# Performance work log

Measured on AMD Instinct MI355X. Metric: run time of the kernel, lower is better.

## Reference

```python
import jax, jax.numpy as jnp
import numpy as np

EMBED = 1024
HEADS = 16
HEAD_DIM = EMBED // HEADS
LN_EPS = 1e-5


def setup_inputs() -> dict:
    key = jax.random.key(0)
    ks = jax.random.split(key, 12)
    B, LQ, LK = 2, 2048, 2048
    s = 1.0 / np.sqrt(EMBED)
    inp = {
        "query_seq": jax.random.normal(ks[0], (B, LQ, EMBED), jnp.float32),
        "key_value_seq": jax.random.normal(ks[1], (B, LK, EMBED), jnp.float32),
        "prompt_size": 0,
        "Wq": jax.random.normal(ks[2], (EMBED, EMBED), jnp.float32) * s,
        "bq": jnp.zeros((EMBED,), jnp.float32),
        "Wk": jax.random.normal(ks[3], (EMBED, EMBED), jnp.float32) * s,
        "bk": jnp.zeros((EMBED,), jnp.float32),
        "Wv": jax.random.normal(ks[4], (EMBED, EMBED), jnp.float32) * s,
        "bv": jnp.zeros((EMBED,), jnp.float32),
        "Wo": jax.random.normal(ks[5], (EMBED, EMBED), jnp.float32) * s,
        "bo": jnp.zeros((EMBED,), jnp.float32),
        "ln_gamma": jnp.ones((EMBED,), jnp.float32),
        "ln_beta": jnp.zeros((EMBED,), jnp.float32),
    }
    return inp


def _split_heads(x):
    B, L, _ = x.shape
    return x.reshape(B, L, HEADS, HEAD_DIM).transpose(0, 2, 1, 3)  # [B,H,L,Dh]


def reference(query_seq, key_value_seq, prompt_size, Wq, bq, Wk, bk, Wv, bv, Wo, bo, ln_gamma, ln_beta):
    # projections (torch nn.Linear: x @ W.T + b)
    q = _split_heads(query_seq @ Wq.T + bq)
    k = _split_heads(key_value_seq @ Wk.T + bk)
    v = _split_heads(key_value_seq @ Wv.T + bv)
    # naive attention: full score matrix, softmax over keys
    scores = jnp.einsum("bhqd,bhkd->bhqk", q, k) / np.sqrt(HEAD_DIM).astype(np.float32)
    attn = jax.nn.softmax(scores, axis=-1)
    ctx = jnp.einsum("bhqk,bhkd->bhqd", attn, v)
    B, H, LQ, Dh = ctx.shape
    ctx = ctx.transpose(0, 2, 1, 3).reshape(B, LQ, H * Dh)
    out = ctx @ Wo.T + bo
    # residual + LayerNorm
    x = out + query_seq
    mu = jnp.mean(x, axis=-1, keepdims=True)
    var = jnp.var(x, axis=-1, keepdims=True)
    return (x - mu) * jax.lax.rsqrt(var + LN_EPS) * ln_gamma + ln_beta
```

## Files before the change

### kernel.cpp

```cpp
#include <hip/hip_runtime.h>

typedef unsigned short u16;
typedef unsigned int u32;
typedef __attribute__((ext_vector_type(8))) __bf16 bf16x8;
typedef __attribute__((ext_vector_type(4))) float f32x4;
typedef __attribute__((ext_vector_type(16))) float f32x16;

#define EMBED 1024
#define NB 2
#define LQ 2048
#define HEADS 16
#define DH 64
#define QSCALE 0.18033688011112042f

__device__ __forceinline__ u16 f2bf(float f) {
  u32 u = __float_as_uint(f);
  u32 r = (u + 0x7FFFu + ((u >> 16) & 1u)) >> 16;
  return (u16)r;
}

__device__ __forceinline__ void glds16(const void* g, void* l) {
  __builtin_amdgcn_global_load_lds((const __attribute__((address_space(1))) void*)g,
                                   (__attribute__((address_space(3))) void*)l, 16, 0, 0);
}

__device__ __forceinline__ f32x4 mfma16(bf16x8 a, bf16x8 b, f32x4 c) {
  return __builtin_amdgcn_mfma_f32_16x16x32_bf16(a, b, c, 0, 0, 0);
}
__device__ __forceinline__ f32x16 mfma32(bf16x8 a, bf16x8 b, f32x16 c) {
  return __builtin_amdgcn_mfma_f32_32x32x16_bf16(a, b, c, 0, 0, 0);
}

__device__ __forceinline__ void pl32(u32& a, u32& b) {
  asm("v_permlane32_swap_b32 %0, %1" : "+v"(a), "+v"(b));
}

__device__ __forceinline__ u32 packbf(float a, float b) {
  return __builtin_amdgcn_perm(__float_as_uint(b), __float_as_uint(a), 0x07060302u);
}

__global__ __launch_bounds__(256) void cast_kernel(
    const float* __restrict__ q, const float* __restrict__ kv,
    const float* __restrict__ wq, const float* __restrict__ wk,
    const float* __restrict__ wv, const float* __restrict__ wo,
    u16* __restrict__ qb, u16* __restrict__ kvb, u16* __restrict__ wqb,
    u16* __restrict__ wkb, u16* __restrict__ wvb, u16* __restrict__ wob) {
  int bid = blockIdx.x;
  const float* src;
  u16* dst;
  long base;
  if (bid < 2048) {
    src = q; dst = qb; base = (long)bid * 2048;
  } else if (bid < 4096) {
    src = kv; dst = kvb; base = (long)(bid - 2048) * 2048;
  } else {
    int wsel = (bid - 4096) >> 9;
    int wb = (bid - 4096) & 511;
    if (wsel == 0) { src = wq; dst = wqb; }
    else if (wsel == 1) { src = wk; dst = wkb; }
    else if (wsel == 2) { src = wv; dst = wvb; }
    else { src = wo; dst = wob; }
    base = (long)wb * 2048;
  }
  long e = base + (long)threadIdx.x * 8;
  float4 f0 = *(const float4*)(src + e);
  float4 f1 = *(const float4*)(src + e + 4);
  uint4 o;
  o.x = (u32)f2bf(f0.x) | ((u32)f2bf(f0.y) << 16);
  o.y = (u32)f2bf(f0.z) | ((u32)f2bf(f0.w) << 16);
  o.z = (u32)f2bf(f1.x) | ((u32)f2bf(f1.y) << 16);
  o.w = (u32)f2bf(f1.z) | ((u32)f2bf(f1.w) << 16);
  *(uint4*)(dst + e) = o;
}

template <int IT>
__device__ __forceinline__ void gemm_core(
    u16* As, u16* Bs, const u16* __restrict__ A, const u16* __restrict__ W,
    const float* __restrict__ bias, const float* __restrict__ resid,
    void* __restrict__ outp, int mode, int bx, int by) {
  const int K = EMBED;
  const int TM = IT * 32;
  const int tid = threadIdx.x;
  const int lane = tid & 63;
  const int wv = tid >> 6;
  const int wm = wv >> 1, wn = wv & 1;
  const int l16 = lane & 15, quad = lane >> 4;
  const long tile_m = (long)bx * TM;
  const long tile_n = (long)by * 128;

  f32x4 z4 = {0.f, 0.f, 0.f, 0.f};
  f32x4 acc[IT][4];
#pragma unroll
  for (int i = 0; i < IT; i++)
#pragma unroll
    for (int j = 0; j < 4; j++) acc[i][j] = z4;

  for (int k0 = 0; k0 < K; k0 += 64) {
#pragma unroll
    for (int it = 0; it < TM / 32; it++) {
      int lin = it * 256 + tid;
      int row = lin >> 3, cc = lin & 7;
      glds16(A + (tile_m + row) * K + k0 + ((cc ^ (row & 7)) << 3), As + lin * 8);
    }
#pragma unroll
    for (int it = 0; it < 4; it++) {
      int lin = it * 256 + tid;
      int row = lin >> 3, cc = lin & 7;
      glds16(W + (tile_n + row) * K + k0 + ((cc ^ (row & 7)) << 3), Bs + lin * 8);
    }
    __syncthreads();
#pragma unroll
    for (int ki = 0; ki < 2; ki++) {
      bf16x8 af[IT], bfr[4];
#pragma unroll
      for (int i = 0; i < IT; i++) {
        int row = wm * (IT * 16) + i * 16 + l16;
        af[i] = *(const bf16x8*)(As + row * 64 + (((ki * 4 + quad) ^ (row & 7)) << 3));
      }
#pragma unroll
      for (int j = 0; j < 4; j++) {
        int row = wn * 64 + j * 16 + l16;
        bfr[j] = *(const bf16x8*)(Bs + row * 64 + (((ki * 4 + quad) ^ (row & 7)) << 3));
      }
#pragma unroll
      for (int i = 0; i < IT; i++)
#pragma unroll
        for (int j = 0; j < 4; j++) acc[i][j] = mfma16(af[i], bfr[j], acc[i][j]);
    }
    __syncthreads();
  }

#pragma unroll
  for (int j = 0; j < 4; j++) {
    int gn = (int)tile_n + wn * 64 + j * 16 + l16;
    float bv = bias[gn];
#pragma unroll
    for (int i = 0; i < IT; i++) {
      long gm0 = tile_m + wm * (IT * 16) + i * 16 + quad * 4;
      if (mode == 3) {
#pragma unroll
        for (int r = 0; r < 4; r++) {
          long idx = (gm0 + r) * EMBED + gn;
          ((float*)outp)[idx] = acc[i][j][r] + bv + resid[idx];
        }
      } else if (mode == 2) {
        int b = (int)(gm0 >> 11), l = (int)(gm0 & 2047);
        int hh = gn >> 6, dh = gn & 63;
        uint2 pk;
        pk.x = (u32)f2bf(acc[i][j][0] + bv) | ((u32)f2bf(acc[i][j][1] + bv) << 16);
        pk.y = (u32)f2bf(acc[i][j][2] + bv) | ((u32)f2bf(acc[i][j][3] + bv) << 16);
        *(uint2*)((u16*)outp + (long)((b * HEADS + hh) * DH + dh) * LQ + l) = pk;
      } else {
#pragma unroll
        for (int r = 0; r < 4; r++) {
          long gm = gm0 + r;
          float v = acc[i][j][r] + bv;
          if (mode == 0) v *= QSCALE;
          int b = (int)(gm >> 11), l = (int)(gm & 2047);
          int hh = gn >> 6, dh = gn & 63;
          ((u16*)outp)[(long)((b * HEADS + hh) * LQ + l) * DH + dh] = f2bf(v);
        }
      }
    }
  }
}

__global__ __launch_bounds__(256, 4) void qkv_kernel(
    const u16* __restrict__ qb, const u16* __restrict__ kvb,
    const u16* __restrict__ wqb, const u16* __restrict__ wkb, const u16* __restrict__ wvb,
    const float* __restrict__ bq, const float* __restrict__ bk, const float* __restrict__ bv,
    u16* __restrict__ Qh, u16* __restrict__ Kh, u16* __restrict__ Vt) {
  __shared__ u16 As[64 * 64];
  __shared__ u16 Bs[128 * 64];
  if (blockIdx.z == 0)      gemm_core<2>(As, Bs, qb,  wqb, bq, nullptr, Qh, 0, blockIdx.x, blockIdx.y);
  else if (blockIdx.z == 1) gemm_core<2>(As, Bs, kvb, wkb, bk, nullptr, Kh, 1, blockIdx.x, blockIdx.y);
  else                      gemm_core<2>(As, Bs, kvb, wvb, bv, nullptr, Vt, 2, blockIdx.x, blockIdx.y);
}

__global__ __launch_bounds__(256, 4) void oproj_kernel(
    const u16* __restrict__ ctx, const u16* __restrict__ wob,
    const float* __restrict__ bo, const float* __restrict__ resid, float* __restrict__ out) {
  __shared__ u16 As[64 * 64];
  __shared__ u16 Bs[128 * 64];
  gemm_core<2>(As, Bs, ctx, wob, bo, resid, out, 3, blockIdx.x, blockIdx.y);
}

__global__ __launch_bounds__(256, 2) void attn_kernel(
    const u16* __restrict__ Qh, const u16* __restrict__ Kh,
    const u16* __restrict__ Vt, u16* __restrict__ ctx) {
  __shared__ u16 KVs[4][2][64 * 64];
  const int tid = threadIdx.x;
  const int lane = tid & 63;
  const int wv = tid >> 6;
  const int l32 = lane & 31, h = lane >> 5;
  const int qt = blockIdx.x, bh = blockIdx.y;
  const long qoff = (long)bh * (LQ * DH) + (long)qt * (128 * DH);
  const long koff = (long)bh * (LQ * DH);
  const long voff = (long)bh * (DH * LQ);
  const int qbase = wv * 32;

#define STAGE_KV(t, N)                                                          \
  do {                                                                          \
    _Pragma("unroll") for (int it = 0; it < 2; it++) {                          \
      int lin = it * 256 + tid;                                                 \
      int row = lin >> 3, cc = lin & 7;                                         \
      glds16(Kh + koff + (long)((t) * 64 + row) * 64 + ((cc ^ (row & 7)) << 3), \
             &KVs[N][0][0] + lin * 8);                                          \
      glds16(Vt + voff + (long)row * LQ + (t) * 64 + ((cc ^ (row & 7)) << 3),   \
             &KVs[N][1][0] + lin * 8);                                          \
    }                                                                           \
  } while (0)

#define SYNC(W)                                                                 \
  do {                                                                          \
    asm volatile("s_waitcnt vmcnt(" #W ")" ::: "memory");                       \
    __builtin_amdgcn_s_barrier();                                               \
    asm volatile("" ::: "memory");                                              \
  } while (0)

  bf16x8 bq[4];
  {
    const u16* qp = Qh + qoff + (qbase + l32) * 64 + h * 8;
#pragma unroll
    for (int ks = 0; ks < 4; ks++) bq[ks] = *(const bf16x8*)(qp + ks * 16);
  }

  STAGE_KV(0, 0);
  STAGE_KV(1, 1);
  STAGE_KV(2, 2);
  SYNC(4);

  f32x16 z16 = {0.f, 0.f, 0.f, 0.f, 0.f, 0.f, 0.f, 0.f,
                0.f, 0.f, 0.f, 0.f, 0.f, 0.f, 0.f, 0.f};
  f32x16 ot[2];
  ot[0] = z16;
  ot[1] = z16;
  f32x16 st[2];
  uint2 pk[2][4];
  float2 ls2 = {0.f, 0.f};

#define DO_S(C)                                                                  \
  do {                                                                           \
    __builtin_amdgcn_s_setprio(1);                                               \
    _Pragma("unroll") for (int ks = 0; ks < 4; ks++) {                           \
      _Pragma("unroll") for (int mt = 0; mt < 2; mt++) {                         \
        int row = mt * 32 + l32;                                                 \
        bf16x8 ak = *(const bf16x8*)(&KVs[C][0][0] + row * 64 +                  \
                                     (((ks * 2 + h) ^ (row & 7)) << 3));         \
        st[mt] = mfma32(ak, bq[ks], (ks == 0) ? z16 : st[mt]);                   \
      }                                                                          \
    }                                                                            \
    __builtin_amdgcn_s_setprio(0);                                               \
  } while (0)

#define DO_SM()                                                                  \
  do {                                                                           \
    _Pragma("unroll") for (int mt = 0; mt < 2; mt++) {                           \
      _Pragma("unroll") for (int g = 0; g < 4; g++) {                            \
        float p0 = __builtin_amdgcn_exp2f(st[mt][g * 4 + 0]);                    \
        float p1 = __builtin_amdgcn_exp2f(st[mt][g * 4 + 1]);                    \
        float p2 = __builtin_amdgcn_exp2f(st[mt][g * 4 + 2]);                    \
        float p3 = __builtin_amdgcn_exp2f(st[mt][g * 4 + 3]);                    \
        ls2.x += p0 + p2;                                                        \
        ls2.y += p1 + p3;                                                        \
        pk[mt][g].x = packbf(p0, p1);                                            \
        pk[mt][g].y = packbf(p2, p3);                                            \
      }                                                                          \
    }                                                                            \
  } while (0)

#define DO_PV(P)                                                                 \
  do {                                                                           \
    _Pragma("unroll") for (int s = 0; s < 4; s++) {                              \
      uint2 wa = pk[s >> 1][(s & 1) * 2];                                        \
      uint2 wb = pk[s >> 1][(s & 1) * 2 + 1];                                    \
      u32 a0 = wa.x, b0 = wb.x, a1 = wa.y, b1 = wb.y;                            \
      pl32(a0, b0);                                                              \
      pl32(a1, b1);                                                              \
      union { u32 u[4]; bf16x8 v; } bp;                                          \
      bp.u[0] = a0;                                                              \
      bp.u[1] = a1;                                                              \
      bp.u[2] = b0;                                                              \
      bp.u[3] = b1;                                                              \
      __builtin_amdgcn_s_setprio(1);                                             \
      _Pragma("unroll") for (int mt2 = 0; mt2 < 2; mt2++) {                      \
        int row = mt2 * 32 + l32;                                                \
        bf16x8 av = *(const bf16x8*)(&KVs[P][1][0] + row * 64 +                  \
                                     ((((s << 1) + h) ^ (row & 7)) << 3));       \
        ot[mt2] = mfma32(av, bp.v, ot[mt2]);                                     \
      }                                                                          \
      __builtin_amdgcn_s_setprio(0);                                             \
    }                                                                            \
  } while (0)

#define AITER(kt, P, C, N, W)                                                    \
  do {                                                                           \
    if ((kt) + 2 < 32) STAGE_KV((kt) + 2, N);                                    \
    DO_SM();                                                                     \
    DO_S(C);                                                                     \
    DO_PV(P);                                                                    \
    SYNC(W);                                                                     \
  } while (0)

  DO_S(0);

  AITER(1, 0, 1, 3, 4);
  for (int k0 = 2; k0 < 30; k0 += 4) {
    AITER(k0 + 0, 1, 2, 0, 4);
    AITER(k0 + 1, 2, 3, 1, 4);
    AITER(k0 + 2, 3, 0, 2, 4);
    AITER(k0 + 3, 0, 1, 3, 4);
  }
  AITER(30, 1, 2, 0, 0);
  AITER(31, 2, 3, 1, 0);
  DO_SM();
  DO_PV(3);

#undef STAGE_KV
#undef SYNC
#undef DO_S
#undef DO_SM
#undef DO_PV
#undef AITER

  float lsum = ls2.x + ls2.y;
  lsum += __shfl_xor(lsum, 32);
  float inv = 1.0f / lsum;

  const int b = bh >> 4, head = bh & 15;
  int qrow = qt * 128 + qbase + l32;
  long base = (long)(b * LQ + qrow) * EMBED + head * DH;
#pragma unroll
  for (int mt = 0; mt < 2; mt++) {
#pragma unroll
    for (int g = 0; g < 4; g++) {
      uint2 pkk;
      pkk.x = (u32)f2bf(ot[mt][g * 4 + 0] * inv) | ((u32)f2bf(ot[mt][g * 4 + 1] * inv) << 16);
      pkk.y = (u32)f2bf(ot[mt][g * 4 + 2] * inv) | ((u32)f2bf(ot[mt][g * 4 + 3] * inv) << 16);
      *(uint2*)(ctx + base + mt * 32 + g * 8 + 4 * h) = pkk;
    }
  }
}

__global__ __launch_bounds__(256) void ln_kernel(
    float* __restrict__ x, const float* __restrict__ gamma, const float* __restrict__ beta) {
  __shared__ float red[8];
  const int tid = threadIdx.x;
  const long row = blockIdx.x;
  float4 v = *(const float4*)(x + row * EMBED + tid * 4);
  float s = v.x + v.y + v.z + v.w;
  float sq = v.x * v.x + v.y * v.y + v.z * v.z + v.w * v.w;
#pragma unroll
  for (int off = 1; off < 64; off <<= 1) {
    s += __shfl_xor(s, off);
    sq += __shfl_xor(sq, off);
  }
  if ((tid & 63) == 0) {
    red[(tid >> 6) * 2] = s;
    red[(tid >> 6) * 2 + 1] = sq;
  }
  __syncthreads();
  s = red[0] + red[2] + red[4] + red[6];
  sq = red[1] + red[3] + red[5] + red[7];
  float mu = s * (1.f / EMBED);
  float var = sq * (1.f / EMBED) - mu * mu;
  float rstd = rsqrtf(var + 1e-5f);
  float4 g = *(const float4*)(gamma + tid * 4);
  float4 bt = *(const float4*)(beta + tid * 4);
  float4 ov;
  ov.x = (v.x - mu) * rstd * g.x + bt.x;
  ov.y = (v.y - mu) * rstd * g.y + bt.y;
  ov.z = (v.z - mu) * rstd * g.z + bt.z;
  ov.w = (v.w - mu) * rstd * g.w + bt.w;
  *(float4*)(x + row * EMBED + tid * 4) = ov;
}

extern "C" void kernel_launch(void* const* d_in, const int* in_sizes, int n_in,
                              void* d_out, int out_size, void* d_ws, size_t ws_size,
                              hipStream_t stream) {
  const float* q     = (const float*)d_in[0];
  const float* kv    = (const float*)d_in[1];
  const float* Wq    = (const float*)d_in[3];
  const float* bq    = (const float*)d_in[4];
  const float* Wk    = (const float*)d_in[5];
  const float* bk    = (const float*)d_in[6];
  const float* Wv    = (const float*)d_in[7];
  const float* bv    = (const float*)d_in[8];
  const float* Wo    = (const float*)d_in[9];
  const float* bo    = (const float*)d_in[10];
  const float* gamma = (const float*)d_in[11];
  const float* beta  = (const float*)d_in[12];

  char* ws = (char*)d_ws;
  u16* qb  = (u16*)(ws + (0l  << 20));
  u16* kvb = (u16*)(ws + (8l  << 20));
  u16* wqb = (u16*)(ws + (16l << 20));
  u16* wkb = (u16*)(ws + (18l << 20));
  u16* wvb = (u16*)(ws + (20l << 20));
  u16* wob = (u16*)(ws + (22l << 20));
  u16* Qh  = (u16*)(ws + (24l << 20));
  u16* Kh  = (u16*)(ws + (32l << 20));
  u16* Vt  = (u16*)(ws + (40l << 20));
  u16* ctx = (u16*)(ws + (48l << 20));
  float* out = (float*)d_out;

  cast_kernel<<<6144, 256, 0, stream>>>(q, kv, Wq, Wk, Wv, Wo, qb, kvb, wqb, wkb, wvb, wob);
  qkv_kernel<<<dim3(64, 8, 3), 256, 0, stream>>>(qb, kvb, wqb, wkb, wvb, bq, bk, bv, Qh, Kh, Vt);
  attn_kernel<<<dim3(16, 32), 256, 0, stream>>>(Qh, Kh, Vt, ctx);
  oproj_kernel<<<dim3(64, 8), 256, 0, stream>>>(ctx, wob, bo, q, out);
  ln_kernel<<<4096, 256, 0, stream>>>(out, gamma, beta);
}
```

Measured before the change: 207.7 us.

## Batch LDS loads and interleave softmax with QK MFMAs in attention loop

The attention inner loop now loads all K and V fragments from LDS into registers up front. It splits the score MFMA and the exp/pack softmax work by half-tile, so exp on one half can overlap MFMAs on the other, and it issues all PV MFMAs back to back. The launch grid is also flattened to 1D with a block-index swizzle, so blocks that land on the same XCD share the same batch-head K/V. This costs more VGPRs for the buffered fragments, which could hurt occupancy at the current launch bounds of 2 blocks per CU.

```diff
diff --git a/kernel.cpp b/kernel.cpp
--- a/kernel.cpp
+++ b/kernel.cpp
@@ -193,7 +193,9 @@
   const int lane = tid & 63;
   const int wv = tid >> 6;
   const int l32 = lane & 31, h = lane >> 5;
-  const int qt = blockIdx.x, bh = blockIdx.y;
+  const int bid = (int)blockIdx.x;
+  const int swz = (bid & 7) * 64 + (bid >> 3);
+  const int bh = swz >> 4, qt = swz & 15;
   const long qoff = (long)bh * (LQ * DH) + (long)qt * (128 * DH);
   const long koff = (long)bh * (LQ * DH);
   const long voff = (long)bh * (DH * LQ);
@@ -237,39 +239,54 @@
   ot[1] = z16;
   f32x16 st[2];
   uint2 pk[2][4];
+  bf16x8 ak[4][2], av[4][2], bpv[4];
   float2 ls2 = {0.f, 0.f};
 
-#define DO_S(C)                                                                  \
-  do {                                                                           \
-    __builtin_amdgcn_s_setprio(1);                                               \
+#define LOAD_K(C)                                                                \
+  do {                                                                           \
     _Pragma("unroll") for (int ks = 0; ks < 4; ks++) {                           \
       _Pragma("unroll") for (int mt = 0; mt < 2; mt++) {                         \
         int row = mt * 32 + l32;                                                 \
-        bf16x8 ak = *(const bf16x8*)(&KVs[C][0][0] + row * 64 +                  \
-                                     (((ks * 2 + h) ^ (row & 7)) << 3));         \
-        st[mt] = mfma32(ak, bq[ks], (ks == 0) ? z16 : st[mt]);                   \
+        ak[ks][mt] = *(const bf16x8*)(&KVs[C][0][0] + row * 64 +                 \
+                                      (((ks * 2 + h) ^ (row & 7)) << 3));        \
       }                                                                          \
     }                                                                            \
-    __builtin_amdgcn_s_setprio(0);                                               \
-  } while (0)
-
-#define DO_SM()                                                                  \
-  do {                                                                           \
-    _Pragma("unroll") for (int mt = 0; mt < 2; mt++) {                           \
-      _Pragma("unroll") for (int g = 0; g < 4; g++) {                            \
-        float p0 = __builtin_amdgcn_exp2f(st[mt][g * 4 + 0]);                    \
-        float p1 = __builtin_amdgcn_exp2f(st[mt][g * 4 + 1]);                    \
-        float p2 = __builtin_amdgcn_exp2f(st[mt][g * 4 + 2]);                    \
-        float p3 = __builtin_amdgcn_exp2f(st[mt][g * 4 + 3]);                    \
-        ls2.x += p0 + p2;                                                        \
-        ls2.y += p1 + p3;                                                        \
-        pk[mt][g].x = packbf(p0, p1);                                            \
-        pk[mt][g].y = packbf(p2, p3);                                            \
+  } while (0)
+
+#define LOAD_V(P)                                                                \
+  do {                                                                           \
+    _Pragma("unroll") for (int s = 0; s < 4; s++) {                              \
+      _Pragma("unroll") for (int mt2 = 0; mt2 < 2; mt2++) {                      \
+        int row = mt2 * 32 + l32;                                                \
+        av[s][mt2] = *(const bf16x8*)(&KVs[P][1][0] + row * 64 +                 \
+                                      ((((s << 1) + h) ^ (row & 7)) << 3));      \
       }                                                                          \
     }                                                                            \
   } while (0)
 
-#define DO_PV(P)                                                                 \
+#define DO_S_H(MT)                                                               \
+  do {                                                                           \
+    __builtin_amdgcn_s_setprio(1);                                               \
+    _Pragma("unroll") for (int ks = 0; ks < 4; ks++)                             \
+        st[MT] = mfma32(ak[ks][MT], bq[ks], (ks == 0) ? z16 : st[MT]);           \
+    __builtin_amdgcn_s_setprio(0);                                               \
+  } while (0)
+
+#define DO_SM_H(MT)                                                              \
+  do {                                                                           \
+    _Pragma("unroll") for (int g = 0; g < 4; g++) {                              \
+      float p0 = __builtin_amdgcn_exp2f(st[MT][g * 4 + 0]);                      \
+      float p1 = __builtin_amdgcn_exp2f(st[MT][g * 4 + 1]);                      \
+      float p2 = __builtin_amdgcn_exp2f(st[MT][g * 4 + 2]);                      \
+      float p3 = __builtin_amdgcn_exp2f(st[MT][g * 4 + 3]);                      \
+      ls2.x += p0 + p2;                                                          \
+      ls2.y += p1 + p3;                                                          \
+      pk[MT][g].x = packbf(p0, p1);                                              \
+      pk[MT][g].y = packbf(p2, p3);                                              \
+    }                                                                            \
+  } while (0)
+
+#define DO_PL()                                                                  \
   do {                                                                           \
     _Pragma("unroll") for (int s = 0; s < 4; s++) {                              \
       uint2 wa = pk[s >> 1][(s & 1) * 2];                                        \
@@ -282,27 +299,37 @@
       bp.u[1] = a1;                                                              \
       bp.u[2] = b0;                                                              \
       bp.u[3] = b1;                                                              \
-      __builtin_amdgcn_s_setprio(1);                                             \
-      _Pragma("unroll") for (int mt2 = 0; mt2 < 2; mt2++) {                      \
-        int row = mt2 * 32 + l32;                                                \
-        bf16x8 av = *(const bf16x8*)(&KVs[P][1][0] + row * 64 +                  \
-                                     ((((s << 1) + h) ^ (row & 7)) << 3));       \
-        ot[mt2] = mfma32(av, bp.v, ot[mt2]);                                     \
-      }                                                                          \
-      __builtin_amdgcn_s_setprio(0);                                             \
+      bpv[s] = bp.v;                                                             \
     }                                                                            \
   } while (0)
 
+#define DO_PV()                                                                  \
+  do {                                                                           \
+    __builtin_amdgcn_s_setprio(1);                                               \
+    _Pragma("unroll") for (int s = 0; s < 4; s++) {                              \
+      _Pragma("unroll") for (int mt2 = 0; mt2 < 2; mt2++)                        \
+          ot[mt2] = mfma32(av[s][mt2], bpv[s], ot[mt2]);                         \
+    }                                                                            \
+    __builtin_amdgcn_s_setprio(0);                                               \
+  } while (0)
+
 #define AITER(kt, P, C, N, W)                                                    \
   do {                                                                           \
     if ((kt) + 2 < 32) STAGE_KV((kt) + 2, N);                                    \
-    DO_SM();                                                                     \
-    DO_S(C);                                                                     \
-    DO_PV(P);                                                                    \
+    LOAD_K(C);                                                                   \
+    DO_SM_H(0);                                                                  \
+    DO_S_H(0);                                                                   \
+    DO_SM_H(1);                                                                  \
+    DO_S_H(1);                                                                   \
+    LOAD_V(P);                                                                   \
+    DO_PL();                                                                     \
+    DO_PV();                                                                     \
     SYNC(W);                                                                     \
   } while (0)
 
-  DO_S(0);
+  LOAD_K(0);
+  DO_S_H(0);
+  DO_S_H(1);
 
   AITER(1, 0, 1, 3, 4);
   for (int k0 = 2; k0 < 30; k0 += 4) {
@@ -313,13 +340,19 @@
   }
   AITER(30, 1, 2, 0, 0);
   AITER(31, 2, 3, 1, 0);
-  DO_SM();
-  DO_PV(3);
+  DO_SM_H(0);
+  DO_SM_H(1);
+  LOAD_V(3);
+  DO_PL();
+  DO_PV();
 
 #undef STAGE_KV
 #undef SYNC
-#undef DO_S
-#undef DO_SM
+#undef LOAD_K
+#undef LOAD_V
+#undef DO_S_H
+#undef DO_SM_H
+#undef DO_PL
 #undef DO_PV
 #undef AITER
 
@@ -406,7 +439,7 @@
 
   cast_kernel<<<6144, 256, 0, stream>>>(q, kv, Wq, Wk, Wv, Wo, qb, kvb, wqb, wkb, wvb, wob);
   qkv_kernel<<<dim3(64, 8, 3), 256, 0, stream>>>(qb, kvb, wqb, wkb, wvb, bq, bk, bv, Qh, Kh, Vt);
-  attn_kernel<<<dim3(16, 32), 256, 0, stream>>>(Qh, Kh, Vt, ctx);
+  attn_kernel<<<512, 256, 0, stream>>>(Qh, Kh, Vt, ctx);
   oproj_kernel<<<dim3(64, 8), 256, 0, stream>>>(ctx, wob, bo, q, out);
   ln_kernel<<<4096, 256, 0, stream>>>(out, gamma, beta);
 }
```

Result: no change. 208.1 us (+0.2%).

## Split attention key tiles across wave pairs and merge partial outputs in LDS

Applied to the files above, without the earlier changes.

The attention kernel now runs 512 threads per block: each pair of waves shares a 32-row query slice, and each wave handles half of every 64-key tile. Each wave computes scores for its 32 keys and accumulates P·V, and the two partial outputs and row sums are combined through LDS at the end. This doubles the waves per block to add latency hiding and halves per-wave score registers. It costs an extra LDS merge with two block barriers and smaller per-wave MFMA work. The block index is also swizzled so consecutive blocks spread across batch-heads.

```diff
diff --git a/kernel.cpp b/kernel.cpp
--- a/kernel.cpp
+++ b/kernel.cpp
@@ -185,30 +185,32 @@
   gemm_core<2>(As, Bs, ctx, wob, bo, resid, out, 3, blockIdx.x, blockIdx.y);
 }
 
-__global__ __launch_bounds__(256, 2) void attn_kernel(
+__global__ __launch_bounds__(512, 4) void attn_kernel(
     const u16* __restrict__ Qh, const u16* __restrict__ Kh,
     const u16* __restrict__ Vt, u16* __restrict__ ctx) {
   __shared__ u16 KVs[4][2][64 * 64];
   const int tid = threadIdx.x;
   const int lane = tid & 63;
   const int wv = tid >> 6;
+  const int qsub = wv >> 1;
+  const int kh = wv & 1;
   const int l32 = lane & 31, h = lane >> 5;
-  const int qt = blockIdx.x, bh = blockIdx.y;
+  const int bid = (int)blockIdx.x;
+  const int swz = (bid & 7) * 64 + (bid >> 3);
+  const int bh = swz >> 4, qt = swz & 15;
   const long qoff = (long)bh * (LQ * DH) + (long)qt * (128 * DH);
   const long koff = (long)bh * (LQ * DH);
   const long voff = (long)bh * (DH * LQ);
-  const int qbase = wv * 32;
+  const int qbase = qsub * 32;
+  const int krow = kh * 32 + l32;
 
 #define STAGE_KV(t, N)                                                          \
   do {                                                                          \
-    _Pragma("unroll") for (int it = 0; it < 2; it++) {                          \
-      int lin = it * 256 + tid;                                                 \
-      int row = lin >> 3, cc = lin & 7;                                         \
-      glds16(Kh + koff + (long)((t) * 64 + row) * 64 + ((cc ^ (row & 7)) << 3), \
-             &KVs[N][0][0] + lin * 8);                                          \
-      glds16(Vt + voff + (long)row * LQ + (t) * 64 + ((cc ^ (row & 7)) << 3),   \
-             &KVs[N][1][0] + lin * 8);                                          \
-    }                                                                           \
+    int row = tid >> 3, cc = tid & 7;                                           \
+    glds16(Kh + koff + (long)((t) * 64 + row) * 64 + ((cc ^ (row & 7)) << 3),   \
+           &KVs[N][0][0] + tid * 8);                                            \
+    glds16(Vt + voff + (long)row * LQ + (t) * 64 + ((cc ^ (row & 7)) << 3),     \
+           &KVs[N][1][0] + tid * 8);                                            \
   } while (0)
 
 #define SYNC(W)                                                                 \
@@ -228,52 +230,47 @@
   STAGE_KV(0, 0);
   STAGE_KV(1, 1);
   STAGE_KV(2, 2);
-  SYNC(4);
+  SYNC(2);
 
   f32x16 z16 = {0.f, 0.f, 0.f, 0.f, 0.f, 0.f, 0.f, 0.f,
                 0.f, 0.f, 0.f, 0.f, 0.f, 0.f, 0.f, 0.f};
   f32x16 ot[2];
   ot[0] = z16;
   ot[1] = z16;
-  f32x16 st[2];
-  uint2 pk[2][4];
+  f32x16 st;
+  uint2 pk[4];
   float2 ls2 = {0.f, 0.f};
 
 #define DO_S(C)                                                                  \
   do {                                                                           \
     __builtin_amdgcn_s_setprio(1);                                               \
     _Pragma("unroll") for (int ks = 0; ks < 4; ks++) {                           \
-      _Pragma("unroll") for (int mt = 0; mt < 2; mt++) {                         \
-        int row = mt * 32 + l32;                                                 \
-        bf16x8 ak = *(const bf16x8*)(&KVs[C][0][0] + row * 64 +                  \
-                                     (((ks * 2 + h) ^ (row & 7)) << 3));         \
-        st[mt] = mfma32(ak, bq[ks], (ks == 0) ? z16 : st[mt]);                   \
-      }                                                                          \
+      bf16x8 ak = *(const bf16x8*)(&KVs[C][0][0] + krow * 64 +                   \
+                                   (((ks * 2 + h) ^ (krow & 7)) << 3));          \
+      st = mfma32(ak, bq[ks], (ks == 0) ? z16 : st);                             \
     }                                                                            \
     __builtin_amdgcn_s_setprio(0);                                               \
   } while (0)
 
 #define DO_SM()                                                                  \
   do {                                                                           \
-    _Pragma("unroll") for (int mt = 0; mt < 2; mt++) {                           \
-      _Pragma("unroll") for (int g = 0; g < 4; g++) {                            \
-        float p0 = __builtin_amdgcn_exp2f(st[mt][g * 4 + 0]);                    \
-        float p1 = __builtin_amdgcn_exp2f(st[mt][g * 4 + 1]);                    \
-        float p2 = __builtin_amdgcn_exp2f(st[mt][g * 4 + 2]);                    \
-        float p3 = __builtin_amdgcn_exp2f(st[mt][g * 4 + 3]);                    \
-        ls2.x += p0 + p2;                                                        \
-        ls2.y += p1 + p3;                                                        \
-        pk[mt][g].x = packbf(p0, p1);                                            \
-        pk[mt][g].y = packbf(p2, p3);                                            \
-      }                                                                          \
+    _Pragma("unroll") for (int g = 0; g < 4; g++) {                              \
+      float p0 = __builtin_amdgcn_exp2f(st[g * 4 + 0]);                          \
+      float p1 = __builtin_amdgcn_exp2f(st[g * 4 + 1]);                          \
+      float p2 = __builtin_amdgcn_exp2f(st[g * 4 + 2]);                          \
+      float p3 = __builtin_amdgcn_exp2f(st[g * 4 + 3]);                          \
+      ls2.x += p0 + p2;                                                          \
+      ls2.y += p1 + p3;                                                          \
+      pk[g].x = packbf(p0, p1);                                                  \
+      pk[g].y = packbf(p2, p3);                                                  \
     }                                                                            \
   } while (0)
 
 #define DO_PV(P)                                                                 \
   do {                                                                           \
-    _Pragma("unroll") for (int s = 0; s < 4; s++) {                              \
-      uint2 wa = pk[s >> 1][(s & 1) * 2];                                        \
-      uint2 wb = pk[s >> 1][(s & 1) * 2 + 1];                                    \
+    _Pragma("unroll") for (int s = 0; s < 2; s++) {                              \
+      uint2 wa = pk[s * 2];                                                      \
+      uint2 wb = pk[s * 2 + 1];                                                  \
       u32 a0 = wa.x, b0 = wb.x, a1 = wa.y, b1 = wb.y;                            \
       pl32(a0, b0);                                                              \
       pl32(a1, b1);                                                              \
@@ -285,8 +282,9 @@
       __builtin_amdgcn_s_setprio(1);                                             \
       _Pragma("unroll") for (int mt2 = 0; mt2 < 2; mt2++) {                      \
         int row = mt2 * 32 + l32;                                                \
+        int c = ((2 * kh + s) << 1) + h;                                         \
         bf16x8 av = *(const bf16x8*)(&KVs[P][1][0] + row * 64 +                  \
-                                     ((((s << 1) + h) ^ (row & 7)) << 3));       \
+                                     ((c ^ (row & 7)) << 3));                    \
         ot[mt2] = mfma32(av, bp.v, ot[mt2]);                                     \
       }                                                                          \
       __builtin_amdgcn_s_setprio(0);                                             \
@@ -304,12 +302,12 @@
 
   DO_S(0);
 
-  AITER(1, 0, 1, 3, 4);
+  AITER(1, 0, 1, 3, 2);
   for (int k0 = 2; k0 < 30; k0 += 4) {
-    AITER(k0 + 0, 1, 2, 0, 4);
-    AITER(k0 + 1, 2, 3, 1, 4);
-    AITER(k0 + 2, 3, 0, 2, 4);
-    AITER(k0 + 3, 0, 1, 3, 4);
+    AITER(k0 + 0, 1, 2, 0, 2);
+    AITER(k0 + 1, 2, 3, 1, 2);
+    AITER(k0 + 2, 3, 0, 2, 2);
+    AITER(k0 + 3, 0, 1, 3, 2);
   }
   AITER(30, 1, 2, 0, 0);
   AITER(31, 2, 3, 1, 0);
@@ -325,19 +323,39 @@
 
   float lsum = ls2.x + ls2.y;
   lsum += __shfl_xor(lsum, 32);
-  float inv = 1.0f / lsum;
-
-  const int b = bh >> 4, head = bh & 15;
-  int qrow = qt * 128 + qbase + l32;
-  long base = (long)(b * LQ + qrow) * EMBED + head * DH;
-#pragma unroll
-  for (int mt = 0; mt < 2; mt++) {
-#pragma unroll
-    for (int g = 0; g < 4; g++) {
-      uint2 pkk;
-      pkk.x = (u32)f2bf(ot[mt][g * 4 + 0] * inv) | ((u32)f2bf(ot[mt][g * 4 + 1] * inv) << 16);
-      pkk.y = (u32)f2bf(ot[mt][g * 4 + 2] * inv) | ((u32)f2bf(ot[mt][g * 4 + 3] * inv) << 16);
-      *(uint2*)(ctx + base + mt * 32 + g * 8 + 4 * h) = pkk;
+
+  float* mrgf = (float*)(&KVs[0][0][0]);
+  float* mlsf = mrgf + 4 * 64 * 36;
+  __syncthreads();
+  if (kh == 1) {
+    int mbase = (qsub * 64 + lane) * 36;
+#pragma unroll
+    for (int mt2 = 0; mt2 < 2; mt2++)
+#pragma unroll
+      for (int e = 0; e < 16; e++) mrgf[mbase + mt2 * 16 + e] = ot[mt2][e];
+    mlsf[qsub * 64 + lane] = lsum;
+  }
+  __syncthreads();
+  if (kh == 0) {
+    int mbase = (qsub * 64 + lane) * 36;
+    lsum += mlsf[qsub * 64 + lane];
+    float inv = 1.0f / lsum;
+    const int b = bh >> 4, head = bh & 15;
+    int qrow = qt * 128 + qbase + l32;
+    long base = (long)(b * LQ + qrow) * EMBED + head * DH;
+#pragma unroll
+    for (int mt2 = 0; mt2 < 2; mt2++) {
+#pragma unroll
+      for (int g = 0; g < 4; g++) {
+        float o0 = (ot[mt2][g * 4 + 0] + mrgf[mbase + mt2 * 16 + g * 4 + 0]) * inv;
+        float o1 = (ot[mt2][g * 4 + 1] + mrgf[mbase + mt2 * 16 + g * 4 + 1]) * inv;
+        float o2 = (ot[mt2][g * 4 + 2] + mrgf[mbase + mt2 * 16 + g * 4 + 2]) * inv;
+        float o3 = (ot[mt2][g * 4 + 3] + mrgf[mbase + mt2 * 16 + g * 4 + 3]) * inv;
+        uint2 pkk;
+        pkk.x = (u32)f2bf(o0) | ((u32)f2bf(o1) << 16);
+        pkk.y = (u32)f2bf(o2) | ((u32)f2bf(o3) << 16);
+        *(uint2*)(ctx + base + mt2 * 32 + g * 8 + 4 * h) = pkk;
+      }
     }
   }
 }
@@ -406,7 +424,7 @@
 
   cast_kernel<<<6144, 256, 0, stream>>>(q, kv, Wq, Wk, Wv, Wo, qb, kvb, wqb, wkb, wvb, wob);
   qkv_kernel<<<dim3(64, 8, 3), 256, 0, stream>>>(qb, kvb, wqb, wkb, wvb, bq, bk, bv, Qh, Kh, Vt);
-  attn_kernel<<<dim3(16, 32), 256, 0, stream>>>(Qh, Kh, Vt, ctx);
+  attn_kernel<<<512, 512, 0, stream>>>(Qh, Kh, Vt, ctx);
   oproj_kernel<<<dim3(64, 8), 256, 0, stream>>>(ctx, wob, bo, q, out);
   ln_kernel<<<4096, 256, 0, stream>>>(out, gamma, beta);
 }
```

Measured after the change: 206.2 us. Within noise of the previous version (-0.7%).
